# Optimization experiments

Measured on AMD Instinct MI355X. Metric: run time of the kernel, lower is better.

The kernel has to match this reference:

```python
import jax, jax.numpy as jnp
import numpy as np


def _gcn_conv(x, W, b, src, dst, n_nodes):
    # PyG GCNConv with add_self_loops=True, edge_weight=None (implicit ones),
    # symmetric normalization: D^{-1/2} A_hat D^{-1/2} (X W) + b
    xw = x @ W                                    # [N, H]
    loop = jnp.arange(n_nodes, dtype=src.dtype)
    src_f = jnp.concatenate([src, loop])          # [E+N]
    dst_f = jnp.concatenate([dst, loop])          # [E+N]
    w = jnp.ones(src_f.shape[0], dtype=x.dtype)
    deg = jax.ops.segment_sum(w, dst_f, num_segments=n_nodes)  # in-degree incl. self-loop
    dinv = jnp.where(deg > 0, jax.lax.rsqrt(deg), 0.0)
    norm = dinv[src_f] * dinv[dst_f]              # [E+N]
    msgs = norm[:, None] * xw[src_f]              # [E+N, H]
    out = jax.ops.segment_sum(msgs, dst_f, num_segments=n_nodes)
    return out + b


def setup_inputs() -> dict:
    key = jax.random.key(0)
    k1, k2, k3, k4 = jax.random.split(key, 4)
    N, E, D, H = 100000, 1600000, 256, 128
    x = jax.random.normal(k1, (N, D), dtype=jnp.float32)
    edge_index = jax.random.randint(k2, (2, E), 0, N, dtype=jnp.int64)
    # Glorot-scaled weights
    W1 = jax.random.normal(k3, (D, H), dtype=jnp.float32) * np.sqrt(2.0 / (D + H))
    b1 = jnp.zeros((H,), dtype=jnp.float32)
    W2 = jax.random.normal(k4, (H, 1), dtype=jnp.float32) * np.sqrt(2.0 / (H + 1))
    b2 = jnp.zeros((1,), dtype=jnp.float32)
    return {"x": x, "edge_index": edge_index, "W1": W1, "b1": b1, "W2": W2, "b2": b2}


def reference(x, edge_index, W1, b1, W2, b2):
    n_nodes = x.shape[0]
    src, dst = edge_index[0], edge_index[1]
    h = _gcn_conv(x, W1, b1, src, dst, n_nodes)   # conv1
    h = jax.nn.relu(h)                            # relu; dropout is identity in eval mode
    out = _gcn_conv(h, W2, b2, src, dst, n_nodes) # conv2 -> [N, 1]
    return out.reshape(-1)                        # x.view(-1)
```

## Files before the change

kernel.cpp:

```cpp
#include <hip/hip_runtime.h>
#include <hip/hip_fp16.h>
#include <cstdint>
#include <cstddef>


#define BSH 9
#define BNODES (1 << BSH)
#define BPAD 16
#define BCAP 9216

typedef _Float16 half8 __attribute__((ext_vector_type(8)));
typedef _Float16 half2t __attribute__((ext_vector_type(2)));
typedef float floatx4 __attribute__((ext_vector_type(4)));
typedef float floatv4 __attribute__((ext_vector_type(4)));
typedef int intv4 __attribute__((ext_vector_type(4)));
typedef unsigned int uintv4 __attribute__((ext_vector_type(4)));

__global__ __launch_bounds__(256) void prep_k(const float* __restrict__ W1,
                                              _Float16* __restrict__ wz,
                                              _Float16* __restrict__ z1h,
                                              float* __restrict__ z2w,
                                              int* __restrict__ cnt,
                                              int* __restrict__ gcur,
                                              int N, int NB) {
  int b = blockIdx.x, tid = threadIdx.x;
  if (b < 128) {
    int id = b * 256 + tid;
    int j = id & 7, lane = (id >> 3) & 63, nb = (id >> 9) & 7, kb = id >> 12;
    int k = kb * 32 + ((lane >> 4) << 3) + j;
    int n = nb * 16 + (lane & 15);
    wz[id] = (_Float16)W1[k * 128 + n];
  } else if (b == 128) {
    if (tid < 128) z1h[(size_t)N * 128 + tid] = (_Float16)0.f;
    if (tid == 0) { z2w[N] = 0.f; cnt[N] = 0; }
  } else {
    int i = (b - 129) * 256 + tid;
    if (i < NB * BPAD) gcur[i] = 0;
  }
}

__global__ __launch_bounds__(256) void stage_k(int kind, int fb, int g0,
                                               const float* __restrict__ X,
                                               const _Float16* __restrict__ wz,
                                               _Float16* __restrict__ z1h, int N,
                                               const int* __restrict__ src,
                                               const int* __restrict__ dst,
                                               int* __restrict__ gcur,
                                               int* __restrict__ barr,
                                               int* __restrict__ ell,
                                               int* __restrict__ ell2,
                                               int* __restrict__ cnt,
                                               int E, int NB) {
  __shared__ char lds_raw[16 * 1024];
  int tid = threadIdx.x;

  if ((int)blockIdx.x < fb) {
    if (kind == 0) {
      int* bc = (int*)lds_raw;
      int* bb = bc + 512;
      for (int i = tid; i < NB; i += 256) bc[i] = 0;
      __syncthreads();
      int base = ((int)blockIdx.x * 256 + tid) * 16;
      int dv[16], sv[16], rv[16], bkv[16];
      int ne = 0;
      if (base + 15 < E) {
#pragma unroll
        for (int q4 = 0; q4 < 4; ++q4) {
          intv4 d4 = __builtin_nontemporal_load((const intv4*)(dst + base + q4 * 4));
          intv4 s4 = __builtin_nontemporal_load((const intv4*)(src + base + q4 * 4));
          dv[q4 * 4 + 0] = d4[0]; dv[q4 * 4 + 1] = d4[1];
          dv[q4 * 4 + 2] = d4[2]; dv[q4 * 4 + 3] = d4[3];
          sv[q4 * 4 + 0] = s4[0]; sv[q4 * 4 + 1] = s4[1];
          sv[q4 * 4 + 2] = s4[2]; sv[q4 * 4 + 3] = s4[3];
        }
        ne = 16;
      } else {
        for (int e = base; e < E && e < base + 16; ++e) {
          dv[ne] = dst[e]; sv[ne] = src[e]; ++ne;
        }
      }
      for (int i = 0; i < ne; ++i) {
        bkv[i] = dv[i] >> BSH;
        rv[i] = atomicAdd(&bc[bkv[i]], 1);
      }
      __syncthreads();
      for (int i = tid; i < NB; i += 256) {
        int cc = bc[i];
        bb[i] = cc ? atomicAdd(&gcur[i * BPAD], cc) : 0;
      }
      __syncthreads();
      for (int i = 0; i < ne; ++i) {
        int pos = bb[bkv[i]] + rv[i];
        if (pos < BCAP) {
          unsigned dl = (unsigned)(dv[i] & (BNODES - 1));
          barr[(size_t)bkv[i] * BCAP + pos] = (int)((dl << 23) | (unsigned)sv[i]);
        }
      }
    } else {
      int* cl = (int*)lds_raw;
      int bkt = (int)blockIdx.x;
      int lo = bkt << BSH;
      for (int i = tid; i < BNODES; i += 256) cl[i] = 0;
      __syncthreads();
      int cb = min(gcur[bkt * BPAD], BCAP);
      const int* seg = barr + (size_t)bkt * BCAP;
      for (int e = tid; e < cb; e += 256) {
        unsigned v = (unsigned)seg[e];
        int dl = (int)(v >> 23);
        int s = (int)(v & 0x7FFFFFu);
        int p = atomicAdd(&cl[dl], 1);
        if (p < 32) ell[(size_t)(lo + dl) * 32 + p] = s;
        else if (p < 63) ell2[(size_t)(lo + dl) * 32 + (p - 32)] = s;
      }
      __syncthreads();
      for (int i = tid; i < BNODES; i += 256) {
        int node = lo + i;
        if (node < N) cnt[node] = cl[i];
      }
    }
    return;
  }

  _Float16* Bl = (_Float16*)lds_raw;
  _Float16* Ol = (_Float16*)lds_raw;

  int wave = tid >> 6, lane = tid & 63;
  int m = lane & 15, q = lane >> 4;
  int row0 = (g0 + (int)blockIdx.x - fb) * 64;
  int row = row0 + wave * 16 + m;

  floatx4 acc[8];
#pragma unroll
  for (int nb = 0; nb < 8; ++nb) acc[nb] = (floatx4)(0.f);

  const uintv4* wsrc = (const uintv4*)wz;
  uintv4* bdst = (uintv4*)Bl;

#pragma unroll
  for (int ph = 0; ph < 4; ++ph) {
    if (ph) __syncthreads();
#pragma unroll
    for (int i = 0; i < 4; ++i) bdst[i * 256 + tid] = wsrc[ph * 1024 + i * 256 + tid];
    __syncthreads();
#pragma unroll
    for (int kk = 0; kk < 2; ++kk) {
      int kb = ph * 2 + kk;
      half8 a;
      if (row < N) {
        const floatv4* ap = (const floatv4*)(X + (size_t)row * 256 + kb * 32 + q * 8);
        floatv4 a0 = __builtin_nontemporal_load(ap);
        floatv4 a1 = __builtin_nontemporal_load(ap + 1);
        a[0] = (_Float16)a0[0]; a[1] = (_Float16)a0[1];
        a[2] = (_Float16)a0[2]; a[3] = (_Float16)a0[3];
        a[4] = (_Float16)a1[0]; a[5] = (_Float16)a1[1];
        a[6] = (_Float16)a1[2]; a[7] = (_Float16)a1[3];
      } else {
#pragma unroll
        for (int j = 0; j < 8; ++j) a[j] = (_Float16)0.f;
      }
#pragma unroll
      for (int nb = 0; nb < 8; ++nb) {
        half8 b = *(const half8*)(Bl + ((size_t)(kk * 8 + nb) * 64 + lane) * 8);
        acc[nb] = __builtin_amdgcn_mfma_f32_16x16x32_f16(a, b, acc[nb], 0, 0, 0);
      }
    }
  }
  __syncthreads();

#pragma unroll
  for (int nb = 0; nb < 8; ++nb) {
    int col = nb * 16 + m;
#pragma unroll
    for (int r = 0; r < 4; ++r) {
      int orow = wave * 16 + q * 4 + r;
      Ol[orow * 128 + col] = (_Float16)acc[nb][r];
    }
  }
  __syncthreads();

  const uintv4* osrc = (const uintv4*)Ol;
  uintv4* gdst = (uintv4*)(z1h + (size_t)row0 * 128);
#pragma unroll
  for (int i = 0; i < 4; ++i) {
    int idx = i * 256 + tid;
    int r = idx >> 4;
    if (row0 + r < N) gdst[idx] = osrc[idx];
  }
}

__global__ __launch_bounds__(256) void agg1_k(const _Float16* __restrict__ z1h,
                                              const int* __restrict__ cnt,
                                              const int* __restrict__ ell,
                                              const int* __restrict__ ell2,
                                              const float* __restrict__ b1,
                                              const float* __restrict__ W2,
                                              float* __restrict__ z2w, int N) {
  int d = blockIdx.x * 4 + (threadIdx.x >> 6);
  int lane = threadIdx.x & 63;
  if (d >= N) return;
  int cd = cnt[d];
  int c = min(cd, 63);
  int ct = c + 1;
  int raw;
  if (c > 32) {
    raw = (lane < 32) ? ell[(size_t)d * 32 + lane]
                      : ell2[(size_t)d * 32 + (lane - 32)];
  } else {
    raw = ell[(size_t)d * 32 + (lane & 31)];
  }
  int up = __shfl_up(raw, 1, 64);
  int idx = (lane == 0) ? d : ((lane < ct) ? up : N);
  float wl = rsqrtf((float)(cnt[idx] + 1));
  float dd = rsqrtf((float)(cd + 1));

  int g = lane >> 4;
  int a8 = (lane & 15) * 8;
  float acc[8];
#pragma unroll
  for (int k = 0; k < 8; ++k) acc[k] = 0.f;

  int t = 0;
  for (; t + 16 <= ct; t += 16) {
    int s0 = __shfl(idx, t + g, 64);
    int s1 = __shfl(idx, t + 4 + g, 64);
    int s2 = __shfl(idx, t + 8 + g, 64);
    int s3 = __shfl(idx, t + 12 + g, 64);
    float w0 = __shfl(wl, t + g, 64);
    float w1 = __shfl(wl, t + 4 + g, 64);
    float w2 = __shfl(wl, t + 8 + g, 64);
    float w3 = __shfl(wl, t + 12 + g, 64);
    half8 v0 = *(const half8*)(z1h + (size_t)s0 * 128 + a8);
    half8 v1 = *(const half8*)(z1h + (size_t)s1 * 128 + a8);
    half8 v2 = *(const half8*)(z1h + (size_t)s2 * 128 + a8);
    half8 v3 = *(const half8*)(z1h + (size_t)s3 * 128 + a8);
#pragma unroll
    for (int k = 0; k < 8; ++k) acc[k] = fmaf(w0, (float)v0[k], acc[k]);
#pragma unroll
    for (int k = 0; k < 8; ++k) acc[k] = fmaf(w1, (float)v1[k], acc[k]);
#pragma unroll
    for (int k = 0; k < 8; ++k) acc[k] = fmaf(w2, (float)v2[k], acc[k]);
#pragma unroll
    for (int k = 0; k < 8; ++k) acc[k] = fmaf(w3, (float)v3[k], acc[k]);
  }
  for (; t < ct; t += 4) {
    int s0 = __shfl(idx, t + g, 64);
    float w0 = __shfl(wl, t + g, 64);
    half8 v0 = *(const half8*)(z1h + (size_t)s0 * 128 + a8);
#pragma unroll
    for (int k = 0; k < 8; ++k) acc[k] = fmaf(w0, (float)v0[k], acc[k]);
  }

#pragma unroll
  for (int k = 0; k < 8; ++k) {
    acc[k] += __shfl_xor(acc[k], 16, 64);
    acc[k] += __shfl_xor(acc[k], 32, 64);
  }

  float4 bA = *(const float4*)(b1 + a8);
  float4 bB = *(const float4*)(b1 + a8 + 4);
  float4 wA = *(const float4*)(W2 + a8);
  float4 wB = *(const float4*)(W2 + a8 + 4);
  float dot = fmaxf(fmaf(dd, acc[0], bA.x), 0.f) * wA.x
            + fmaxf(fmaf(dd, acc[1], bA.y), 0.f) * wA.y
            + fmaxf(fmaf(dd, acc[2], bA.z), 0.f) * wA.z
            + fmaxf(fmaf(dd, acc[3], bA.w), 0.f) * wA.w
            + fmaxf(fmaf(dd, acc[4], bB.x), 0.f) * wB.x
            + fmaxf(fmaf(dd, acc[5], bB.y), 0.f) * wB.y
            + fmaxf(fmaf(dd, acc[6], bB.z), 0.f) * wB.z
            + fmaxf(fmaf(dd, acc[7], bB.w), 0.f) * wB.w;
#pragma unroll
  for (int off = 8; off >= 1; off >>= 1) dot += __shfl_xor(dot, off, 64);
  if (lane == 0) z2w[d] = dd * dot;
}

__global__ __launch_bounds__(256) void agg2_k(const float* __restrict__ z2w,
                                              const int* __restrict__ cnt,
                                              const int* __restrict__ ell,
                                              const int* __restrict__ ell2,
                                              const float* __restrict__ b2,
                                              float* __restrict__ out, int N) {
  int wv = threadIdx.x >> 6;
  int half = (threadIdx.x >> 5) & 1;
  int j = threadIdx.x & 31;
  int d = blockIdx.x * 8 + wv * 2 + half;
  if (d >= N) return;
  int cd = cnt[d];
  int c = min(cd, 63);
  int raw = ell[(size_t)d * 32 + j];
  int idx = (j < min(c, 32)) ? raw : N;
  float v = z2w[idx];
  if (c > 32 && j < c - 32) v += z2w[ell2[(size_t)d * 32 + j]];
#pragma unroll
  for (int off = 16; off >= 1; off >>= 1) v += __shfl_xor(v, off, 64);
  if (j == 0) out[d] = rsqrtf((float)(cd + 1)) * (v + z2w[d]) + b2[0];
}

extern "C" void kernel_launch(void* const* d_in, const int* in_sizes, int n_in,
                              void* d_out, int out_size, void* d_ws, size_t ws_size,
                              hipStream_t stream) {
  (void)n_in; (void)out_size; (void)ws_size;
  const float* x = (const float*)d_in[0];
  const int* edge = (const int*)d_in[1];
  const float* W1 = (const float*)d_in[2];
  const float* b1 = (const float*)d_in[3];
  const float* W2 = (const float*)d_in[4];
  const float* b2 = (const float*)d_in[5];
  float* out = (float*)d_out;

  const int D = 256, H = 128;
  int N = in_sizes[0] / D;
  int E = in_sizes[1] / 2;
  const int* srcp = edge;
  const int* dstp = edge + E;
  int NB = (N + BNODES - 1) >> BSH;

  char* ws = (char*)d_ws;
  size_t off = 0;
  auto alloc = [&](size_t bytes) -> void* {
    void* p = ws + off;
    off += (bytes + 255) & ~(size_t)255;
    return p;
  };
  int* cnt        = (int*)alloc((size_t)(N + 1) * 4);
  float* z2w      = (float*)alloc((size_t)(N + 1) * 4);
  int* ell        = (int*)alloc((size_t)N * 32 * 4);
  int* ell2       = (int*)alloc((size_t)N * 32 * 4);
  _Float16* wz    = (_Float16*)alloc((size_t)32768 * 2);
  _Float16* z1h   = (_Float16*)alloc((size_t)(N + 1) * H * 2);
  int* gcur       = (int*)alloc((size_t)NB * BPAD * 4);
  int* barr       = (int*)alloc((size_t)NB * BCAP * 4);

  int tiles = (N + 63) / 64;
  int fbA = (E + 4095) / 4096;
  int fbB = NB;

  prep_k<<<dim3(129 + (NB * BPAD + 255) / 256), dim3(256), 0, stream>>>(
      W1, wz, z1h, z2w, cnt, gcur, N, NB);
  stage_k<<<dim3(fbA + tiles), dim3(256), 0, stream>>>(0, fbA, 0, x, wz, z1h, N,
      srcp, dstp, gcur, barr, ell, ell2, cnt, E, NB);
  stage_k<<<dim3(fbB), dim3(256), 0, stream>>>(1, fbB, tiles, x, wz, z1h, N,
      srcp, dstp, gcur, barr, ell, ell2, cnt, E, NB);
  agg1_k<<<dim3((N + 3) / 4), dim3(256), 0, stream>>>(z1h, cnt, ell, ell2, b1, W2, z2w, N);
  agg2_k<<<dim3((N + 7) / 8), dim3(256), 0, stream>>>(z2w, cnt, ell, ell2, b2, out, N);
}
```

Measured before the change: 276.0 us.

## Store self-loop in ELL slot zero and use fma_mix, bpermute, swizzle reductions

The self-loop is now written into the first ELL slot and counts start at one, so aggregation no longer needs a shuffle-up plus a separate self-term, and agg2 drops its extra z2w[d] load. The agg1 inner loop converts fp16 to fp32 inside the multiply-add using inline v_fma_mix_f32, computes gather addresses with byte-offset arithmetic, and uses ds_bpermute and ds_swizzle in place of generic shuffles. The aim is fewer conversion, address and cross-lane instructions in the gather-bound aggregation. In exchange, nodes with high degree now keep one fewer neighbor within the 63-entry cap, and the inline asm depends on the target ISA.

```diff
diff --git a/kernel.cpp b/kernel.cpp
--- a/kernel.cpp
+++ b/kernel.cpp
@@ -10,11 +10,32 @@
 #define BCAP 9216
 
 typedef _Float16 half8 __attribute__((ext_vector_type(8)));
-typedef _Float16 half2t __attribute__((ext_vector_type(2)));
 typedef float floatx4 __attribute__((ext_vector_type(4)));
 typedef float floatv4 __attribute__((ext_vector_type(4)));
 typedef int intv4 __attribute__((ext_vector_type(4)));
 typedef unsigned int uintv4 __attribute__((ext_vector_type(4)));
+
+__device__ __forceinline__ void fmamix8(float (&acc)[8], uint4 v, float w) {
+  asm("v_fma_mix_f32 %0, %1, %2, %0 op_sel:[0,0,0] op_sel_hi:[0,1,0]"
+      : "+v"(acc[0]) : "v"(w), "v"(v.x));
+  asm("v_fma_mix_f32 %0, %1, %2, %0 op_sel:[0,1,0] op_sel_hi:[0,1,0]"
+      : "+v"(acc[1]) : "v"(w), "v"(v.x));
+  asm("v_fma_mix_f32 %0, %1, %2, %0 op_sel:[0,0,0] op_sel_hi:[0,1,0]"
+      : "+v"(acc[2]) : "v"(w), "v"(v.y));
+  asm("v_fma_mix_f32 %0, %1, %2, %0 op_sel:[0,1,0] op_sel_hi:[0,1,0]"
+      : "+v"(acc[3]) : "v"(w), "v"(v.y));
+  asm("v_fma_mix_f32 %0, %1, %2, %0 op_sel:[0,0,0] op_sel_hi:[0,1,0]"
+      : "+v"(acc[4]) : "v"(w), "v"(v.z));
+  asm("v_fma_mix_f32 %0, %1, %2, %0 op_sel:[0,1,0] op_sel_hi:[0,1,0]"
+      : "+v"(acc[5]) : "v"(w), "v"(v.z));
+  asm("v_fma_mix_f32 %0, %1, %2, %0 op_sel:[0,0,0] op_sel_hi:[0,1,0]"
+      : "+v"(acc[6]) : "v"(w), "v"(v.w));
+  asm("v_fma_mix_f32 %0, %1, %2, %0 op_sel:[0,1,0] op_sel_hi:[0,1,0]"
+      : "+v"(acc[7]) : "v"(w), "v"(v.w));
+}
+
+#define SWZF(v, imm) \
+  __int_as_float(__builtin_amdgcn_ds_swizzle(__float_as_int(v), imm))
 
 __global__ __launch_bounds__(256) void prep_k(const float* __restrict__ W1,
                                               _Float16* __restrict__ wz,
@@ -32,7 +53,7 @@
     wz[id] = (_Float16)W1[k * 128 + n];
   } else if (b == 128) {
     if (tid < 128) z1h[(size_t)N * 128 + tid] = (_Float16)0.f;
-    if (tid == 0) { z2w[N] = 0.f; cnt[N] = 0; }
+    if (tid == 0) { z2w[N] = 0.f; cnt[N] = 1; }
   } else {
     int i = (b - 129) * 256 + tid;
     if (i < NB * BPAD) gcur[i] = 0;
@@ -100,7 +121,11 @@
       int* cl = (int*)lds_raw;
       int bkt = (int)blockIdx.x;
       int lo = bkt << BSH;
-      for (int i = tid; i < BNODES; i += 256) cl[i] = 0;
+      for (int i = tid; i < BNODES; i += 256) {
+        cl[i] = 1;
+        int node = lo + i;
+        if (node < N) ell[(size_t)node * 32] = node;
+      }
       __syncthreads();
       int cb = min(gcur[bkt * BPAD], BCAP);
       const int* seg = barr + (size_t)bkt * BCAP;
@@ -198,64 +223,65 @@
   int d = blockIdx.x * 4 + (threadIdx.x >> 6);
   int lane = threadIdx.x & 63;
   if (d >= N) return;
-  int cd = cnt[d];
-  int c = min(cd, 63);
-  int ct = c + 1;
+  int cntd = cnt[d];
+  int ct = min(cntd, 63);
   int raw;
-  if (c > 32) {
+  if (ct > 32) {
     raw = (lane < 32) ? ell[(size_t)d * 32 + lane]
-                      : ell2[(size_t)d * 32 + (lane - 32)];
+                      : (lane < 63 ? ell2[(size_t)d * 32 + (lane - 32)] : N);
   } else {
     raw = ell[(size_t)d * 32 + (lane & 31)];
   }
-  int up = __shfl_up(raw, 1, 64);
-  int idx = (lane == 0) ? d : ((lane < ct) ? up : N);
-  float wl = rsqrtf((float)(cnt[idx] + 1));
-  float dd = rsqrtf((float)(cd + 1));
+  int idx = (lane < ct) ? raw : N;
+  float wl = rsqrtf((float)cnt[idx]);
+  float dd = rsqrtf((float)cntd);
+  int iw = __float_as_int(wl);
 
   int g = lane >> 4;
-  int a8 = (lane & 15) * 8;
-  float acc[8];
-#pragma unroll
-  for (int k = 0; k < 8; ++k) acc[k] = 0.f;
+  unsigned a16 = (unsigned)(lane & 15) << 4;
+  const char* zb = (const char*)z1h;
+  int pa = g << 2;
+  int ax = (lane ^ 32) << 2;
+
+  float acc[8] = {0.f, 0.f, 0.f, 0.f, 0.f, 0.f, 0.f, 0.f};
 
   int t = 0;
   for (; t + 16 <= ct; t += 16) {
-    int s0 = __shfl(idx, t + g, 64);
-    int s1 = __shfl(idx, t + 4 + g, 64);
-    int s2 = __shfl(idx, t + 8 + g, 64);
-    int s3 = __shfl(idx, t + 12 + g, 64);
-    float w0 = __shfl(wl, t + g, 64);
-    float w1 = __shfl(wl, t + 4 + g, 64);
-    float w2 = __shfl(wl, t + 8 + g, 64);
-    float w3 = __shfl(wl, t + 12 + g, 64);
-    half8 v0 = *(const half8*)(z1h + (size_t)s0 * 128 + a8);
-    half8 v1 = *(const half8*)(z1h + (size_t)s1 * 128 + a8);
-    half8 v2 = *(const half8*)(z1h + (size_t)s2 * 128 + a8);
-    half8 v3 = *(const half8*)(z1h + (size_t)s3 * 128 + a8);
-#pragma unroll
-    for (int k = 0; k < 8; ++k) acc[k] = fmaf(w0, (float)v0[k], acc[k]);
-#pragma unroll
-    for (int k = 0; k < 8; ++k) acc[k] = fmaf(w1, (float)v1[k], acc[k]);
-#pragma unroll
-    for (int k = 0; k < 8; ++k) acc[k] = fmaf(w2, (float)v2[k], acc[k]);
-#pragma unroll
-    for (int k = 0; k < 8; ++k) acc[k] = fmaf(w3, (float)v3[k], acc[k]);
+    int a0 = pa + (t << 2);
+    int s0 = __builtin_amdgcn_ds_bpermute(a0, idx);
+    int s1 = __builtin_amdgcn_ds_bpermute(a0 + 16, idx);
+    int s2 = __builtin_amdgcn_ds_bpermute(a0 + 32, idx);
+    int s3 = __builtin_amdgcn_ds_bpermute(a0 + 48, idx);
+    float w0 = __int_as_float(__builtin_amdgcn_ds_bpermute(a0, iw));
+    float w1 = __int_as_float(__builtin_amdgcn_ds_bpermute(a0 + 16, iw));
+    float w2 = __int_as_float(__builtin_amdgcn_ds_bpermute(a0 + 32, iw));
+    float w3 = __int_as_float(__builtin_amdgcn_ds_bpermute(a0 + 48, iw));
+    uint4 v0 = *(const uint4*)(zb + (((unsigned)s0 << 8) + a16));
+    uint4 v1 = *(const uint4*)(zb + (((unsigned)s1 << 8) + a16));
+    uint4 v2 = *(const uint4*)(zb + (((unsigned)s2 << 8) + a16));
+    uint4 v3 = *(const uint4*)(zb + (((unsigned)s3 << 8) + a16));
+    fmamix8(acc, v0, w0);
+    fmamix8(acc, v1, w1);
+    fmamix8(acc, v2, w2);
+    fmamix8(acc, v3, w3);
   }
   for (; t < ct; t += 4) {
-    int s0 = __shfl(idx, t + g, 64);
-    float w0 = __shfl(wl, t + g, 64);
-    half8 v0 = *(const half8*)(z1h + (size_t)s0 * 128 + a8);
-#pragma unroll
-    for (int k = 0; k < 8; ++k) acc[k] = fmaf(w0, (float)v0[k], acc[k]);
+    int a0 = pa + (t << 2);
+    int s0 = __builtin_amdgcn_ds_bpermute(a0, idx);
+    float w0 = __int_as_float(__builtin_amdgcn_ds_bpermute(a0, iw));
+    uint4 v0 = *(const uint4*)(zb + (((unsigned)s0 << 8) + a16));
+    fmamix8(acc, v0, w0);
   }
 
 #pragma unroll
   for (int k = 0; k < 8; ++k) {
-    acc[k] += __shfl_xor(acc[k], 16, 64);
-    acc[k] += __shfl_xor(acc[k], 32, 64);
-  }
-
+    float x = acc[k];
+    x += SWZF(x, 0x401F);
+    x += __int_as_float(__builtin_amdgcn_ds_bpermute(ax, __float_as_int(x)));
+    acc[k] = x;
+  }
+
+  int a8 = (lane & 15) * 8;
   float4 bA = *(const float4*)(b1 + a8);
   float4 bB = *(const float4*)(b1 + a8 + 4);
   float4 wA = *(const float4*)(W2 + a8);
@@ -268,8 +294,10 @@
             + fmaxf(fmaf(dd, acc[5], bB.y), 0.f) * wB.y
             + fmaxf(fmaf(dd, acc[6], bB.z), 0.f) * wB.z
             + fmaxf(fmaf(dd, acc[7], bB.w), 0.f) * wB.w;
-#pragma unroll
-  for (int off = 8; off >= 1; off >>= 1) dot += __shfl_xor(dot, off, 64);
+  dot += SWZF(dot, 0x201F);
+  dot += SWZF(dot, 0x101F);
+  dot += SWZF(dot, 0x081F);
+  dot += SWZF(dot, 0x041F);
   if (lane == 0) z2w[d] = dd * dot;
 }
 
@@ -292,7 +320,7 @@
   if (c > 32 && j < c - 32) v += z2w[ell2[(size_t)d * 32 + j]];
 #pragma unroll
   for (int off = 16; off >= 1; off >>= 1) v += __shfl_xor(v, off, 64);
-  if (j == 0) out[d] = rsqrtf((float)(cd + 1)) * (v + z2w[d]) + b2[0];
+  if (j == 0) out[d] = rsqrtf((float)cd) * v + b2[0];
 }
 
 extern "C" void kernel_launch(void* const* d_in, const int* in_sizes, int n_in,
```

New measurement: 279.6 us. About the same (+1.3%).
